# Kernel tuning notes

Measured on AMD Instinct MI355X. Metric: run time of the kernel, lower is better.

Reference implementation:

```python
import jax, jax.numpy as jnp
import numpy as np

NUM_STEPS = 32
BETA = 0.9
THRESHOLD = 1.0   # LIF firing threshold
LAT_THR = 0.01    # snntorch spikegen.latency default threshold
EPS = 1e-7        # snntorch epsilon
SLOPE = 25.0      # fast_sigmoid surrogate slope
ENC_THR = 0.75    # SpikeEncoder latency_threshold

B, S, F_IN = 512, 64, 128
HIDDEN = [256, 256, 128]


def spike_fn(u):
    # Heaviside forward; surrogate grad handled in fwdbwd module. Forward-only here.
    return (u > 0).astype(u.dtype)


def latency_encode(x, num_steps):
    """SpikeEncoder('latency') -> snntorch.spikegen.latency, normalize=True, linear=False."""
    # gate small values
    x = jnp.where(x < ENC_THR, jnp.zeros_like(x), x)
    # per-channel min-max normalization over the sequence dim (dim=1)
    x_min = jnp.min(x, axis=1, keepdims=True)
    x_max = jnp.max(x, axis=1, keepdims=True)
    xn = (x - x_min) / (x_max - x_min + 1e-8)
    # logarithmic latency code (tau=1, first_spike_time=0, normalize=True)
    d = jnp.clip(xn, LAT_THR + EPS, None)
    t = jnp.log(d / (d - LAT_THR))
    t_max = np.log((LAT_THR + EPS) / EPS)  # spike time of smallest intensity
    t = t * (num_steps - 1) / np.float32(t_max)
    t_idx = jnp.clip(jnp.round(t), 0, num_steps - 1).astype(jnp.int32)  # (B,S,F)
    # one-hot over time -> (T, B, S, F), matches spikegen scatter
    steps = jnp.arange(num_steps, dtype=jnp.int32).reshape(-1, 1, 1, 1)
    return (steps == t_idx[None]).astype(jnp.float32)


def snn_block(x, W, b, beta, thr):
    """Linear over all timesteps, then LIF (reset-by-subtraction) via scan.
    x: (T, B, in) -> spk: (T, B, hidden)"""
    cur = jnp.einsum('tbi,hi->tbh', x, W) + b

    def step(mem, c):
        # snntorch Leaky: reset computed from previous mem (detached)
        reset = jax.lax.stop_gradient((mem - thr > 0).astype(mem.dtype))
        mem = beta * mem + c - reset * thr
        spk = spike_fn(mem - thr)
        return mem, spk

    mem0 = jnp.zeros(cur.shape[1:], cur.dtype)
    _, spk = jax.lax.scan(step, cur[0] * 0 + mem0, cur)
    return spk


def setup_inputs() -> dict:
    key = jax.random.key(0)
    ks = jax.random.split(key, 7)
    x = jax.random.normal(ks[0], (B, S, F_IN), dtype=jnp.float32)
    sizes = [F_IN] + HIDDEN
    params = {}
    for i in range(3):
        fan_in = sizes[i]
        bound = 1.0 / np.sqrt(fan_in)
        params[f'W{i+1}'] = jax.random.uniform(ks[2 * i + 1], (sizes[i + 1], fan_in),
                                               minval=-bound, maxval=bound, dtype=jnp.float32)
        params[f'b{i+1}'] = jax.random.uniform(ks[2 * i + 2], (sizes[i + 1],),
                                               minval=-bound, maxval=bound, dtype=jnp.float32)
    return {'x': x, **params}


def reference(x, W1, b1, W2, b2, W3, b3):
    spikes = latency_encode(x, NUM_STEPS)        # (T, B, S, F)
    spikes = spikes.mean(axis=2)                 # (T, B, F)
    spikes = snn_block(spikes, W1, b1, BETA, THRESHOLD)
    spikes = snn_block(spikes, W2, b2, BETA, THRESHOLD)
    spikes = snn_block(spikes, W3, b3, BETA, THRESHOLD)
    return spikes                                # (T, B, hidden_sizes[-1])
```

## Files before the change

kernel.cpp:

```cpp
#include <hip/hip_runtime.h>
#include <cstddef>

#define T_STEPS 32
#define B_SZ    512
#define S_SZ    64
#define F_INPUT 128
#define H1      256
#define H2      256
#define H3      128

typedef _Float16 half_t;
typedef __attribute__((ext_vector_type(8))) _Float16 half8;
typedef __attribute__((ext_vector_type(4))) float   float4v;

__device__ inline void split_store_sw(float w, half_t* out, int n, int k, int kchunks) {
    half_t hi = (half_t)w;
    float hif = (float)hi;
    if (fabsf(hif) < 6.103515625e-05f) { hi = (half_t)0.0f; hif = 0.0f; }
    half_t lo = (half_t)((w - hif) * 4096.0f);
    int n_tile = n >> 4, lr = n & 15;
    int k_chunk = k >> 5, kin = k & 31, quad = kin >> 3, j = kin & 7;
    size_t base = (size_t)(n_tile * kchunks + k_chunk) * 1024;
    size_t off  = base + (size_t)((quad << 4) + lr) * 8 + j;
    out[off]       = hi;
    out[off + 512] = lo;
}

__global__ __launch_bounds__(256)
void prep_w_kernel(const float* __restrict__ W1, const float* __restrict__ W2,
                   const float* __restrict__ W3,
                   half_t* __restrict__ ws1, half_t* __restrict__ ws2,
                   half_t* __restrict__ ws3) {
    int e = blockIdx.x * blockDim.x + threadIdx.x;
    if (e < H1 * F_INPUT) {
        split_store_sw(W1[e], ws1, e / F_INPUT, e % F_INPUT, F_INPUT / 32);
    } else if (e < H1 * F_INPUT + H2 * H1) {
        int i = e - H1 * F_INPUT;
        split_store_sw(W2[i], ws2, i / H1, i % H1, H1 / 32);
    } else {
        int i = e - H1 * F_INPUT - H2 * H1;
        split_store_sw(W3[i], ws3, i / H2, i % H2, H2 / 32);
    }
}

#define CUR_STRIDE 260
#define AS_STRIDE  136
#define SPK_STRIDE 264
#define SMEM_CUR   0
#define SMEM_AS    33280
#define SMEM_SPK   33280
#define SMEM_TOTAL 50176

template<int KCHUNKS, int NT, int ASTRIDE>
__device__ __forceinline__ void gemm_phase(const half_t* __restrict__ Wsw,
                                           const float*  __restrict__ bias,
                                           const half_t* __restrict__ Als,
                                           float* __restrict__ curT,
                                           int wave, int lane) {
    const int quad = lane >> 4, lr = lane & 15;
    float4v acc_h[2][NT], acc_l[2][NT];
#pragma unroll
    for (int mt = 0; mt < 2; ++mt)
#pragma unroll
        for (int nt = 0; nt < NT; ++nt) {
            acc_h[mt][nt] = (float4v){0.0f, 0.0f, 0.0f, 0.0f};
            acc_l[mt][nt] = (float4v){0.0f, 0.0f, 0.0f, 0.0f};
        }

    half8 wh[NT], wl[NT];
#pragma unroll
    for (int nt = 0; nt < NT; ++nt) {
        const half_t* p = Wsw + ((size_t)(wave * NT + nt) * KCHUNKS) * 1024 + lane * 8;
        wh[nt] = *(const half8*)(p);
        wl[nt] = *(const half8*)(p + 512);
    }

#pragma unroll
    for (int c = 0; c < KCHUNKS; ++c) {
        half8 a0 = *(const half8*)(Als + lr * ASTRIDE        + c * 32 + quad * 8);
        half8 a1 = *(const half8*)(Als + (16 + lr) * ASTRIDE + c * 32 + quad * 8);
        half8 nwh[NT], nwl[NT];
        if (c + 1 < KCHUNKS) {
#pragma unroll
            for (int nt = 0; nt < NT; ++nt) {
                const half_t* p =
                    Wsw + ((size_t)(wave * NT + nt) * KCHUNKS + c + 1) * 1024 + lane * 8;
                nwh[nt] = *(const half8*)(p);
                nwl[nt] = *(const half8*)(p + 512);
            }
        }
#pragma unroll
        for (int nt = 0; nt < NT; ++nt) {
            acc_h[0][nt] = __builtin_amdgcn_mfma_f32_16x16x32_f16(a0, wh[nt], acc_h[0][nt], 0, 0, 0);
            acc_h[1][nt] = __builtin_amdgcn_mfma_f32_16x16x32_f16(a1, wh[nt], acc_h[1][nt], 0, 0, 0);
            acc_l[0][nt] = __builtin_amdgcn_mfma_f32_16x16x32_f16(a0, wl[nt], acc_l[0][nt], 0, 0, 0);
            acc_l[1][nt] = __builtin_amdgcn_mfma_f32_16x16x32_f16(a1, wl[nt], acc_l[1][nt], 0, 0, 0);
        }
#pragma unroll
        for (int nt = 0; nt < NT; ++nt) { wh[nt] = nwh[nt]; wl[nt] = nwl[nt]; }
    }

#pragma unroll
    for (int nt = 0; nt < NT; ++nt) {
        int col = wave * NT * 16 + nt * 16 + lr;
        float bj = bias[col];
#pragma unroll
        for (int mt = 0; mt < 2; ++mt) {
            int rbase = mt * 16 + quad * 4;
#pragma unroll
            for (int r = 0; r < 4; ++r) {
                float v = acc_h[mt][nt][r] + 2.44140625e-04f * acc_l[mt][nt][r];
                curT[(rbase + r) * CUR_STRIDE + col] = v + bj;
            }
        }
    }
}

__global__ __launch_bounds__(512, 4)
void snn_mega_kernel(const float* __restrict__ x,
                     const half_t* __restrict__ ws1, const float* __restrict__ b1,
                     const half_t* __restrict__ ws2, const float* __restrict__ b2,
                     const half_t* __restrict__ ws3, const float* __restrict__ b3,
                     float* __restrict__ out) {
    __shared__ __align__(16) char smem[SMEM_TOTAL];
    float*  curT = (float*) (smem + SMEM_CUR);
    half_t* As   = (half_t*)(smem + SMEM_AS);
    half_t* spk  = (half_t*)(smem + SMEM_SPK);

    const int tid  = threadIdx.x;
    const int b    = blockIdx.x;
    const int wave = tid >> 6;
    const int lane = tid & 63;

    const int f  = tid & 127;
    const int sh = (tid >> 7) & 1;
    const float* xp = x + (size_t)b * (S_SZ * F_INPUT) + (size_t)sh * 32 * F_INPUT + f;
    float* scratch = curT;

    float v[32];
    if (tid < 256) {
#pragma unroll
        for (int s = 0; s < 32; ++s) {
            float val = xp[(size_t)s * F_INPUT];
            v[s] = (val < 0.75f) ? 0.0f : val;
        }
        float mn = 1e30f, mx = -1e30f;
#pragma unroll
        for (int s = 0; s < 32; ++s) {
            mn = fminf(mn, v[s]);
            mx = fmaxf(mx, v[s]);
        }
        scratch[sh * 128 + f]       = mn;
        scratch[256 + sh * 128 + f] = mx;
    }
    __syncthreads();
    float fmn = fminf(scratch[f], scratch[128 + f]);
    float fmx = fmaxf(scratch[256 + f], scratch[384 + f]);
    __syncthreads();

    if (tid < 256) {
        float* hist = scratch;
#pragma unroll
        for (int t = 0; t < T_STEPS; ++t) hist[sh * 4096 + t * 128 + f] = 0.0f;
        const float denom = fmx - fmn + 1e-8f;
#pragma unroll
        for (int s = 0; s < 32; ++s) {
            float g = v[s];
            float xn = (g - fmn) / denom;
            float d  = fmaxf(xn, 0.0100001f);
            float tt = logf(d / (d - 0.01f));
            tt = tt * 31.0f;
            tt = tt / 11.512935464920229f;
            float tr = rintf(tt);
            tr = fminf(fmaxf(tr, 0.0f), 31.0f);
            hist[sh * 4096 + (int)tr * 128 + f] += 1.0f;
        }
    }
    __syncthreads();

#pragma unroll
    for (int i = 0; i < 8; ++i) {
        int idx = tid + i * 512;
        int t = idx >> 7, ff = idx & 127;
        float cnt = scratch[t * 128 + ff] + scratch[4096 + t * 128 + ff];
        As[t * AS_STRIDE + ff] = (half_t)(cnt * 0.015625f);
    }
    __syncthreads();

    gemm_phase<F_INPUT / 32, 2, AS_STRIDE>(ws1, b1, As, curT, wave, lane);
    __syncthreads();
    if (tid < 256) {
#pragma clang fp contract(off)
        const int h = tid;
        float mem = 0.0f;
#pragma unroll
        for (int t = 0; t < T_STEPS; ++t) {
            float c = curT[t * CUR_STRIDE + h];
            float reset = (mem - 1.0f > 0.0f) ? 1.0f : 0.0f;
            float p = 0.9f * mem;
            p = p + c;
            mem = p - reset;
            spk[t * SPK_STRIDE + h] = (half_t)((mem - 1.0f > 0.0f) ? 1.0f : 0.0f);
        }
    }
    __syncthreads();

    gemm_phase<H1 / 32, 2, SPK_STRIDE>(ws2, b2, spk, curT, wave, lane);
    __syncthreads();
    if (tid < 256) {
#pragma clang fp contract(off)
        const int h = tid;
        float mem = 0.0f;
#pragma unroll
        for (int t = 0; t < T_STEPS; ++t) {
            float c = curT[t * CUR_STRIDE + h];
            float reset = (mem - 1.0f > 0.0f) ? 1.0f : 0.0f;
            float p = 0.9f * mem;
            p = p + c;
            mem = p - reset;
            spk[t * SPK_STRIDE + h] = (half_t)((mem - 1.0f > 0.0f) ? 1.0f : 0.0f);
        }
    }
    __syncthreads();

    gemm_phase<H2 / 32, 1, SPK_STRIDE>(ws3, b3, spk, curT, wave, lane);
    __syncthreads();
    if (tid < H3) {
#pragma clang fp contract(off)
        const int h = tid;
        float mem = 0.0f;
#pragma unroll
        for (int t = 0; t < T_STEPS; ++t) {
            float c = curT[t * CUR_STRIDE + h];
            float reset = (mem - 1.0f > 0.0f) ? 1.0f : 0.0f;
            float p = 0.9f * mem;
            p = p + c;
            mem = p - reset;
            out[((size_t)t * B_SZ + b) * H3 + h] = (mem - 1.0f > 0.0f) ? 1.0f : 0.0f;
        }
    }
}

extern "C" void kernel_launch(void* const* d_in, const int* in_sizes, int n_in,
                              void* d_out, int out_size, void* d_ws, size_t ws_size,
                              hipStream_t stream) {
    const float* x  = (const float*)d_in[0];
    const float* W1 = (const float*)d_in[1];
    const float* b1 = (const float*)d_in[2];
    const float* W2 = (const float*)d_in[3];
    const float* b2 = (const float*)d_in[4];
    const float* W3 = (const float*)d_in[5];
    const float* b3 = (const float*)d_in[6];
    float* out = (float*)d_out;

    char* ws = (char*)d_ws;
    half_t* ws1 = (half_t*)ws;
    half_t* ws2 = (half_t*)(ws + 128 * 1024);
    half_t* ws3 = (half_t*)(ws + 384 * 1024);

    prep_w_kernel<<<(H1 * F_INPUT + H2 * H1 + H3 * H2) / 256, 256, 0, stream>>>(
        W1, W2, W3, ws1, ws2, ws3);

    snn_mega_kernel<<<B_SZ, 512, 0, stream>>>(x, ws1, b1, ws2, b2, ws3, b3, out);
}
```

Baseline: 96.83 us.

## Split fused mega-kernel into encode and per-layer GEMM+LIF kernels

Replaces the single per-batch mega-kernel with an encode kernel plus three GEMM+LIF kernels. Each GEMM kernel splits the hidden dimension across two blocks, so layers 1 and 2 launch twice as many blocks, and it uses smaller shared-memory tiles. The goal is more parallelism and occupancy and fewer idle threads in the LIF and encode phases. In exchange it adds kernel-launch overhead and global-memory round trips for the rates and spike tensors between layers.

After: 111.4 us. +15.0%, slower.

```diff
diff --git a/kernel.cpp b/kernel.cpp
--- a/kernel.cpp
+++ b/kernel.cpp
@@ -43,67 +43,141 @@
     }
 }
 
-#define CUR_STRIDE 260
-#define AS_STRIDE  136
-#define SPK_STRIDE 264
-#define SMEM_CUR   0
-#define SMEM_AS    33280
-#define SMEM_SPK   33280
-#define SMEM_TOTAL 50176
-
-template<int KCHUNKS, int NT, int ASTRIDE>
-__device__ __forceinline__ void gemm_phase(const half_t* __restrict__ Wsw,
-                                           const float*  __restrict__ bias,
-                                           const half_t* __restrict__ Als,
-                                           float* __restrict__ curT,
-                                           int wave, int lane) {
+__global__ __launch_bounds__(256)
+void encode_kernel(const float* __restrict__ x, half_t* __restrict__ rates) {
+    __shared__ float scratch[8192];
+    const int tid = threadIdx.x;
+    const int b   = blockIdx.x;
+    const int f   = tid & 127;
+    const int sh  = tid >> 7;
+    const float* xp = x + (size_t)b * (S_SZ * F_INPUT) + (size_t)sh * 32 * F_INPUT + f;
+
+    float v[32];
+#pragma unroll
+    for (int s = 0; s < 32; ++s) {
+        float val = xp[(size_t)s * F_INPUT];
+        v[s] = (val < 0.75f) ? 0.0f : val;
+    }
+    float mn = 1e30f, mx = -1e30f;
+#pragma unroll
+    for (int s = 0; s < 32; ++s) {
+        mn = fminf(mn, v[s]);
+        mx = fmaxf(mx, v[s]);
+    }
+    scratch[sh * 128 + f]       = mn;
+    scratch[256 + sh * 128 + f] = mx;
+    __syncthreads();
+    float fmn = fminf(scratch[f], scratch[128 + f]);
+    float fmx = fmaxf(scratch[256 + f], scratch[384 + f]);
+    __syncthreads();
+
+#pragma unroll
+    for (int t = 0; t < T_STEPS; ++t) scratch[sh * 4096 + t * 128 + f] = 0.0f;
+    const float denom = fmx - fmn + 1e-8f;
+#pragma unroll
+    for (int s = 0; s < 32; ++s) {
+        float g  = v[s];
+        float xn = (g - fmn) / denom;
+        float d  = fmaxf(xn, 0.0100001f);
+        float tt = logf(d / (d - 0.01f));
+        tt = tt * 31.0f;
+        tt = tt / 11.512935464920229f;
+        float tr = rintf(tt);
+        tr = fminf(fmaxf(tr, 0.0f), 31.0f);
+        scratch[sh * 4096 + (int)tr * 128 + f] += 1.0f;
+    }
+    __syncthreads();
+
+#pragma unroll
+    for (int i = 0; i < 16; ++i) {
+        int idx = tid + i * 256;
+        int t = idx >> 7, ff = idx & 127;
+        float cnt = scratch[t * 128 + ff] + scratch[4096 + t * 128 + ff];
+        rates[((size_t)b * T_STEPS + t) * F_INPUT + ff] = (half_t)(cnt * 0.015625f);
+    }
+}
+
+#define CUR_STRIDE 132
+#define SMEM_AS_MAX 16896
+#define SMEM_GEMM  (SMEM_AS_MAX + 32 * CUR_STRIDE * 4)
+
+template<int KCH, int FINAL>
+__global__ __launch_bounds__(256)
+void gemm_lif(const half_t* __restrict__ A,
+              const half_t* __restrict__ Wsw,
+              const float*  __restrict__ bias,
+              half_t* __restrict__ spk_next,
+              float*  __restrict__ out_final,
+              int Nfull) {
+    constexpr int K = KCH * 32;
+    constexpr int ASTRIDE = K + 8;
+    __shared__ __align__(16) char smem[SMEM_GEMM];
+    half_t* As   = (half_t*)smem;
+    float*  curT = (float*)(smem + SMEM_AS_MAX);
+
+    const int tid  = threadIdx.x;
+    const int b    = blockIdx.x;
+    const int n0   = blockIdx.y * 128;
+    const int wave = tid >> 6;
+    const int lane = tid & 63;
     const int quad = lane >> 4, lr = lane & 15;
-    float4v acc_h[2][NT], acc_l[2][NT];
+
+#pragma unroll
+    for (int i = 0; i < KCH / 2; ++i) {
+        int idx  = i * 256 + tid;
+        int row  = idx / (KCH * 4);
+        int colh = (idx % (KCH * 4)) * 8;
+        *(uint4*)(&As[row * ASTRIDE + colh]) =
+            *(const uint4*)(A + ((size_t)b * 32 + row) * K + colh);
+    }
+    __syncthreads();
+
+    float4v acc_h[2][2], acc_l[2][2];
 #pragma unroll
     for (int mt = 0; mt < 2; ++mt)
 #pragma unroll
-        for (int nt = 0; nt < NT; ++nt) {
+        for (int nt = 0; nt < 2; ++nt) {
             acc_h[mt][nt] = (float4v){0.0f, 0.0f, 0.0f, 0.0f};
             acc_l[mt][nt] = (float4v){0.0f, 0.0f, 0.0f, 0.0f};
         }
-
-    half8 wh[NT], wl[NT];
-#pragma unroll
-    for (int nt = 0; nt < NT; ++nt) {
-        const half_t* p = Wsw + ((size_t)(wave * NT + nt) * KCHUNKS) * 1024 + lane * 8;
+    const int ntile0 = (n0 >> 4) + wave * 2;
+
+    half8 wh[2], wl[2];
+#pragma unroll
+    for (int nt = 0; nt < 2; ++nt) {
+        const half_t* p = Wsw + ((size_t)(ntile0 + nt) * KCH) * 1024 + lane * 8;
         wh[nt] = *(const half8*)(p);
         wl[nt] = *(const half8*)(p + 512);
     }
-
-#pragma unroll
-    for (int c = 0; c < KCHUNKS; ++c) {
-        half8 a0 = *(const half8*)(Als + lr * ASTRIDE        + c * 32 + quad * 8);
-        half8 a1 = *(const half8*)(Als + (16 + lr) * ASTRIDE + c * 32 + quad * 8);
-        half8 nwh[NT], nwl[NT];
-        if (c + 1 < KCHUNKS) {
-#pragma unroll
-            for (int nt = 0; nt < NT; ++nt) {
+#pragma unroll
+    for (int c = 0; c < KCH; ++c) {
+        half8 a0 = *(const half8*)(&As[lr * ASTRIDE        + c * 32 + quad * 8]);
+        half8 a1 = *(const half8*)(&As[(16 + lr) * ASTRIDE + c * 32 + quad * 8]);
+        half8 nwh[2], nwl[2];
+        if (c + 1 < KCH) {
+#pragma unroll
+            for (int nt = 0; nt < 2; ++nt) {
                 const half_t* p =
-                    Wsw + ((size_t)(wave * NT + nt) * KCHUNKS + c + 1) * 1024 + lane * 8;
+                    Wsw + ((size_t)(ntile0 + nt) * KCH + c + 1) * 1024 + lane * 8;
                 nwh[nt] = *(const half8*)(p);
                 nwl[nt] = *(const half8*)(p + 512);
             }
         }
 #pragma unroll
-        for (int nt = 0; nt < NT; ++nt) {
+        for (int nt = 0; nt < 2; ++nt) {
             acc_h[0][nt] = __builtin_amdgcn_mfma_f32_16x16x32_f16(a0, wh[nt], acc_h[0][nt], 0, 0, 0);
             acc_h[1][nt] = __builtin_amdgcn_mfma_f32_16x16x32_f16(a1, wh[nt], acc_h[1][nt], 0, 0, 0);
             acc_l[0][nt] = __builtin_amdgcn_mfma_f32_16x16x32_f16(a0, wl[nt], acc_l[0][nt], 0, 0, 0);
             acc_l[1][nt] = __builtin_amdgcn_mfma_f32_16x16x32_f16(a1, wl[nt], acc_l[1][nt], 0, 0, 0);
         }
 #pragma unroll
-        for (int nt = 0; nt < NT; ++nt) { wh[nt] = nwh[nt]; wl[nt] = nwl[nt]; }
-    }
-
-#pragma unroll
-    for (int nt = 0; nt < NT; ++nt) {
-        int col = wave * NT * 16 + nt * 16 + lr;
-        float bj = bias[col];
+        for (int nt = 0; nt < 2; ++nt) { wh[nt] = nwh[nt]; wl[nt] = nwl[nt]; }
+    }
+
+#pragma unroll
+    for (int nt = 0; nt < 2; ++nt) {
+        int col = (wave * 2 + nt) * 16 + lr;
+        float bj = bias[n0 + col];
 #pragma unroll
         for (int mt = 0; mt < 2; ++mt) {
             int rbase = mt * 16 + quad * 4;
@@ -114,82 +188,9 @@
             }
         }
     }
-}
-
-__global__ __launch_bounds__(512, 4)
-void snn_mega_kernel(const float* __restrict__ x,
-                     const half_t* __restrict__ ws1, const float* __restrict__ b1,
-                     const half_t* __restrict__ ws2, const float* __restrict__ b2,
-                     const half_t* __restrict__ ws3, const float* __restrict__ b3,
-                     float* __restrict__ out) {
-    __shared__ __align__(16) char smem[SMEM_TOTAL];
-    float*  curT = (float*) (smem + SMEM_CUR);
-    half_t* As   = (half_t*)(smem + SMEM_AS);
-    half_t* spk  = (half_t*)(smem + SMEM_SPK);
-
-    const int tid  = threadIdx.x;
-    const int b    = blockIdx.x;
-    const int wave = tid >> 6;
-    const int lane = tid & 63;
-
-    const int f  = tid & 127;
-    const int sh = (tid >> 7) & 1;
-    const float* xp = x + (size_t)b * (S_SZ * F_INPUT) + (size_t)sh * 32 * F_INPUT + f;
-    float* scratch = curT;
-
-    float v[32];
-    if (tid < 256) {
-#pragma unroll
-        for (int s = 0; s < 32; ++s) {
-            float val = xp[(size_t)s * F_INPUT];
-            v[s] = (val < 0.75f) ? 0.0f : val;
-        }
-        float mn = 1e30f, mx = -1e30f;
-#pragma unroll
-        for (int s = 0; s < 32; ++s) {
-            mn = fminf(mn, v[s]);
-            mx = fmaxf(mx, v[s]);
-        }
-        scratch[sh * 128 + f]       = mn;
-        scratch[256 + sh * 128 + f] = mx;
-    }
-    __syncthreads();
-    float fmn = fminf(scratch[f], scratch[128 + f]);
-    float fmx = fmaxf(scratch[256 + f], scratch[384 + f]);
-    __syncthreads();
-
-    if (tid < 256) {
-        float* hist = scratch;
-#pragma unroll
-        for (int t = 0; t < T_STEPS; ++t) hist[sh * 4096 + t * 128 + f] = 0.0f;
-        const float denom = fmx - fmn + 1e-8f;
-#pragma unroll
-        for (int s = 0; s < 32; ++s) {
-            float g = v[s];
-            float xn = (g - fmn) / denom;
-            float d  = fmaxf(xn, 0.0100001f);
-            float tt = logf(d / (d - 0.01f));
-            tt = tt * 31.0f;
-            tt = tt / 11.512935464920229f;
-            float tr = rintf(tt);
-            tr = fminf(fmaxf(tr, 0.0f), 31.0f);
-            hist[sh * 4096 + (int)tr * 128 + f] += 1.0f;
-        }
-    }
-    __syncthreads();
-
-#pragma unroll
-    for (int i = 0; i < 8; ++i) {
-        int idx = tid + i * 512;
-        int t = idx >> 7, ff = idx & 127;
-        float cnt = scratch[t * 128 + ff] + scratch[4096 + t * 128 + ff];
-        As[t * AS_STRIDE + ff] = (half_t)(cnt * 0.015625f);
-    }
-    __syncthreads();
-
-    gemm_phase<F_INPUT / 32, 2, AS_STRIDE>(ws1, b1, As, curT, wave, lane);
-    __syncthreads();
-    if (tid < 256) {
+    __syncthreads();
+
+    if (tid < 128) {
 #pragma clang fp contract(off)
         const int h = tid;
         float mem = 0.0f;
@@ -200,43 +201,12 @@
             float p = 0.9f * mem;
             p = p + c;
             mem = p - reset;
-            spk[t * SPK_STRIDE + h] = (half_t)((mem - 1.0f > 0.0f) ? 1.0f : 0.0f);
-        }
-    }
-    __syncthreads();
-
-    gemm_phase<H1 / 32, 2, SPK_STRIDE>(ws2, b2, spk, curT, wave, lane);
-    __syncthreads();
-    if (tid < 256) {
-#pragma clang fp contract(off)
-        const int h = tid;
-        float mem = 0.0f;
-#pragma unroll
-        for (int t = 0; t < T_STEPS; ++t) {
-            float c = curT[t * CUR_STRIDE + h];
-            float reset = (mem - 1.0f > 0.0f) ? 1.0f : 0.0f;
-            float p = 0.9f * mem;
-            p = p + c;
-            mem = p - reset;
-            spk[t * SPK_STRIDE + h] = (half_t)((mem - 1.0f > 0.0f) ? 1.0f : 0.0f);
-        }
-    }
-    __syncthreads();
-
-    gemm_phase<H2 / 32, 1, SPK_STRIDE>(ws3, b3, spk, curT, wave, lane);
-    __syncthreads();
-    if (tid < H3) {
-#pragma clang fp contract(off)
-        const int h = tid;
-        float mem = 0.0f;
-#pragma unroll
-        for (int t = 0; t < T_STEPS; ++t) {
-            float c = curT[t * CUR_STRIDE + h];
-            float reset = (mem - 1.0f > 0.0f) ? 1.0f : 0.0f;
-            float p = 0.9f * mem;
-            p = p + c;
-            mem = p - reset;
-            out[((size_t)t * B_SZ + b) * H3 + h] = (mem - 1.0f > 0.0f) ? 1.0f : 0.0f;
+            float s = (mem - 1.0f > 0.0f) ? 1.0f : 0.0f;
+            if (FINAL) {
+                out_final[((size_t)t * B_SZ + b) * H3 + h] = s;
+            } else {
+                spk_next[((size_t)b * T_STEPS + t) * Nfull + n0 + h] = (half_t)s;
+            }
         }
     }
 }
@@ -254,12 +224,24 @@
     float* out = (float*)d_out;
 
     char* ws = (char*)d_ws;
-    half_t* ws1 = (half_t*)ws;
-    half_t* ws2 = (half_t*)(ws + 128 * 1024);
-    half_t* ws3 = (half_t*)(ws + 384 * 1024);
+    half_t* ws1   = (half_t*)ws;
+    half_t* ws2   = (half_t*)(ws + 128 * 1024);
+    half_t* ws3   = (half_t*)(ws + 384 * 1024);
+    half_t* rates = (half_t*)(ws + (size_t) 1 * 1024 * 1024);
+    half_t* spk1  = (half_t*)(ws + (size_t) 5 * 1024 * 1024);
+    half_t* spk2  = (half_t*)(ws + (size_t)13 * 1024 * 1024);
 
     prep_w_kernel<<<(H1 * F_INPUT + H2 * H1 + H3 * H2) / 256, 256, 0, stream>>>(
         W1, W2, W3, ws1, ws2, ws3);
 
-    snn_mega_kernel<<<B_SZ, 512, 0, stream>>>(x, ws1, b1, ws2, b2, ws3, b3, out);
-}
+    encode_kernel<<<B_SZ, 256, 0, stream>>>(x, rates);
+
+    gemm_lif<4, 0><<<dim3(B_SZ, 2), 256, 0, stream>>>(
+        rates, ws1, b1, spk1, nullptr, H1);
+
+    gemm_lif<8, 0><<<dim3(B_SZ, 2), 256, 0, stream>>>(
+        spk1, ws2, b2, spk2, nullptr, H2);
+
+    gemm_lif<8, 1><<<dim3(B_SZ, 1), 256, 0, stream>>>(
+        spk2, ws3, b3, nullptr, out, H3);
+}
```

## Fuse LIF scan into each wave's GEMM epilogue and drop barriers

Applied to the files above, without the earlier changes.

Each wave now runs the LIF recurrence over the columns it just wrote, so the block-wide barrier between each GEMM and its scan goes away. Separate ping-pong spike buffers (spkA/spkB) replace the single shared spike buffer, and shared memory grows from about 49KB to about 74KB. With larger LDS use, fewer blocks may fit per CU. Only 32 or 16 lanes per wave do the serial scan, so lane utilization during the scan is low.

Measured after the change: 97.08 us. About the same (+0.3%).

```diff
diff --git a/kernel.cpp b/kernel.cpp
--- a/kernel.cpp
+++ b/kernel.cpp
@@ -43,20 +43,23 @@
     }
 }
 
-#define CUR_STRIDE 260
 #define AS_STRIDE  136
 #define SPK_STRIDE 264
-#define SMEM_CUR   0
-#define SMEM_AS    33280
-#define SMEM_SPK   33280
-#define SMEM_TOTAL 50176
-
-template<int KCHUNKS, int NT, int ASTRIDE>
-__device__ __forceinline__ void gemm_phase(const half_t* __restrict__ Wsw,
-                                           const float*  __restrict__ bias,
-                                           const half_t* __restrict__ Als,
-                                           float* __restrict__ curT,
-                                           int wave, int lane) {
+#define CUR_STRIDE 260
+#define SMEM_AS    0
+#define SMEM_CUR   8704
+#define SMEM_SPKA  41984
+#define SMEM_SPKB  58880
+#define SMEM_TOTAL 75776
+
+template<int KCHUNKS, int NT, int ASTRIDE, int FINAL>
+__device__ __forceinline__ void gemm_lif_wave(const half_t* __restrict__ Wsw,
+                                              const float*  __restrict__ bias,
+                                              const half_t* __restrict__ Als,
+                                              float*  __restrict__ curT,
+                                              half_t* __restrict__ spk_out,
+                                              float*  __restrict__ out_final,
+                                              int b, int wave, int lane) {
     const int quad = lane >> 4, lr = lane & 15;
     float4v acc_h[2][NT], acc_l[2][NT];
 #pragma unroll
@@ -74,11 +77,12 @@
         wh[nt] = *(const half8*)(p);
         wl[nt] = *(const half8*)(p + 512);
     }
-
 #pragma unroll
     for (int c = 0; c < KCHUNKS; ++c) {
-        half8 a0 = *(const half8*)(Als + lr * ASTRIDE        + c * 32 + quad * 8);
-        half8 a1 = *(const half8*)(Als + (16 + lr) * ASTRIDE + c * 32 + quad * 8);
+        half8 a[2];
+#pragma unroll
+        for (int mt = 0; mt < 2; ++mt)
+            a[mt] = *(const half8*)(Als + (mt * 16 + lr) * ASTRIDE + c * 32 + quad * 8);
         half8 nwh[NT], nwl[NT];
         if (c + 1 < KCHUNKS) {
 #pragma unroll
@@ -90,19 +94,19 @@
             }
         }
 #pragma unroll
-        for (int nt = 0; nt < NT; ++nt) {
-            acc_h[0][nt] = __builtin_amdgcn_mfma_f32_16x16x32_f16(a0, wh[nt], acc_h[0][nt], 0, 0, 0);
-            acc_h[1][nt] = __builtin_amdgcn_mfma_f32_16x16x32_f16(a1, wh[nt], acc_h[1][nt], 0, 0, 0);
-            acc_l[0][nt] = __builtin_amdgcn_mfma_f32_16x16x32_f16(a0, wl[nt], acc_l[0][nt], 0, 0, 0);
-            acc_l[1][nt] = __builtin_amdgcn_mfma_f32_16x16x32_f16(a1, wl[nt], acc_l[1][nt], 0, 0, 0);
-        }
+        for (int nt = 0; nt < NT; ++nt)
+#pragma unroll
+            for (int mt = 0; mt < 2; ++mt) {
+                acc_h[mt][nt] = __builtin_amdgcn_mfma_f32_16x16x32_f16(a[mt], wh[nt], acc_h[mt][nt], 0, 0, 0);
+                acc_l[mt][nt] = __builtin_amdgcn_mfma_f32_16x16x32_f16(a[mt], wl[nt], acc_l[mt][nt], 0, 0, 0);
+            }
 #pragma unroll
         for (int nt = 0; nt < NT; ++nt) { wh[nt] = nwh[nt]; wl[nt] = nwl[nt]; }
     }
 
 #pragma unroll
     for (int nt = 0; nt < NT; ++nt) {
-        int col = wave * NT * 16 + nt * 16 + lr;
+        int col = (wave * NT + nt) * 16 + lr;
         float bj = bias[col];
 #pragma unroll
         for (int mt = 0; mt < 2; ++mt) {
@@ -111,6 +115,26 @@
             for (int r = 0; r < 4; ++r) {
                 float v = acc_h[mt][nt][r] + 2.44140625e-04f * acc_l[mt][nt][r];
                 curT[(rbase + r) * CUR_STRIDE + col] = v + bj;
+            }
+        }
+    }
+
+    if (lane < NT * 16) {
+#pragma clang fp contract(off)
+        const int col = wave * NT * 16 + lane;
+        float mem = 0.0f;
+#pragma unroll
+        for (int t = 0; t < T_STEPS; ++t) {
+            float c = curT[t * CUR_STRIDE + col];
+            float reset = (mem - 1.0f > 0.0f) ? 1.0f : 0.0f;
+            float p = 0.9f * mem;
+            p = p + c;
+            mem = p - reset;
+            float s = (mem - 1.0f > 0.0f) ? 1.0f : 0.0f;
+            if (FINAL) {
+                out_final[((size_t)t * B_SZ + b) * H3 + col] = s;
+            } else {
+                spk_out[t * SPK_STRIDE + col] = (half_t)s;
             }
         }
     }
@@ -123,9 +147,11 @@
                      const half_t* __restrict__ ws3, const float* __restrict__ b3,
                      float* __restrict__ out) {
     __shared__ __align__(16) char smem[SMEM_TOTAL];
+    half_t* As   = (half_t*)(smem + SMEM_AS);
     float*  curT = (float*) (smem + SMEM_CUR);
-    half_t* As   = (half_t*)(smem + SMEM_AS);
-    half_t* spk  = (half_t*)(smem + SMEM_SPK);
+    half_t* spkA = (half_t*)(smem + SMEM_SPKA);
+    half_t* spkB = (half_t*)(smem + SMEM_SPKB);
+    float*  scratch = (float*)(smem + SMEM_CUR);
 
     const int tid  = threadIdx.x;
     const int b    = blockIdx.x;
@@ -135,9 +161,9 @@
     const int f  = tid & 127;
     const int sh = (tid >> 7) & 1;
     const float* xp = x + (size_t)b * (S_SZ * F_INPUT) + (size_t)sh * 32 * F_INPUT + f;
-    float* scratch = curT;
 
     float v[32];
+    float fmn = 0.0f, fmx = 0.0f;
     if (tid < 256) {
 #pragma unroll
         for (int s = 0; s < 32; ++s) {
@@ -154,8 +180,10 @@
         scratch[256 + sh * 128 + f] = mx;
     }
     __syncthreads();
-    float fmn = fminf(scratch[f], scratch[128 + f]);
-    float fmx = fmaxf(scratch[256 + f], scratch[384 + f]);
+    if (tid < 256) {
+        fmn = fminf(scratch[f], scratch[128 + f]);
+        fmx = fmaxf(scratch[256 + f], scratch[384 + f]);
+    }
     __syncthreads();
 
     if (tid < 256) {
@@ -165,7 +193,7 @@
         const float denom = fmx - fmn + 1e-8f;
 #pragma unroll
         for (int s = 0; s < 32; ++s) {
-            float g = v[s];
+            float g  = v[s];
             float xn = (g - fmn) / denom;
             float d  = fmaxf(xn, 0.0100001f);
             float tt = logf(d / (d - 0.01f));
@@ -178,67 +206,27 @@
     }
     __syncthreads();
 
-#pragma unroll
-    for (int i = 0; i < 8; ++i) {
-        int idx = tid + i * 512;
-        int t = idx >> 7, ff = idx & 127;
-        float cnt = scratch[t * 128 + ff] + scratch[4096 + t * 128 + ff];
-        As[t * AS_STRIDE + ff] = (half_t)(cnt * 0.015625f);
-    }
-    __syncthreads();
-
-    gemm_phase<F_INPUT / 32, 2, AS_STRIDE>(ws1, b1, As, curT, wave, lane);
-    __syncthreads();
-    if (tid < 256) {
-#pragma clang fp contract(off)
-        const int h = tid;
-        float mem = 0.0f;
-#pragma unroll
-        for (int t = 0; t < T_STEPS; ++t) {
-            float c = curT[t * CUR_STRIDE + h];
-            float reset = (mem - 1.0f > 0.0f) ? 1.0f : 0.0f;
-            float p = 0.9f * mem;
-            p = p + c;
-            mem = p - reset;
-            spk[t * SPK_STRIDE + h] = (half_t)((mem - 1.0f > 0.0f) ? 1.0f : 0.0f);
-        }
-    }
-    __syncthreads();
-
-    gemm_phase<H1 / 32, 2, SPK_STRIDE>(ws2, b2, spk, curT, wave, lane);
-    __syncthreads();
-    if (tid < 256) {
-#pragma clang fp contract(off)
-        const int h = tid;
-        float mem = 0.0f;
-#pragma unroll
-        for (int t = 0; t < T_STEPS; ++t) {
-            float c = curT[t * CUR_STRIDE + h];
-            float reset = (mem - 1.0f > 0.0f) ? 1.0f : 0.0f;
-            float p = 0.9f * mem;
-            p = p + c;
-            mem = p - reset;
-            spk[t * SPK_STRIDE + h] = (half_t)((mem - 1.0f > 0.0f) ? 1.0f : 0.0f);
-        }
-    }
-    __syncthreads();
-
-    gemm_phase<H2 / 32, 1, SPK_STRIDE>(ws3, b3, spk, curT, wave, lane);
-    __syncthreads();
-    if (tid < H3) {
-#pragma clang fp contract(off)
-        const int h = tid;
-        float mem = 0.0f;
-#pragma unroll
-        for (int t = 0; t < T_STEPS; ++t) {
-            float c = curT[t * CUR_STRIDE + h];
-            float reset = (mem - 1.0f > 0.0f) ? 1.0f : 0.0f;
-            float p = 0.9f * mem;
-            p = p + c;
-            mem = p - reset;
-            out[((size_t)t * B_SZ + b) * H3 + h] = (mem - 1.0f > 0.0f) ? 1.0f : 0.0f;
-        }
-    }
+    if (tid < 256) {
+#pragma unroll
+        for (int i = 0; i < 16; ++i) {
+            int idx = tid + i * 256;
+            int t = idx >> 7, ff = idx & 127;
+            float cnt = scratch[t * 128 + ff] + scratch[4096 + t * 128 + ff];
+            As[t * AS_STRIDE + ff] = (half_t)(cnt * 0.015625f);
+        }
+    }
+    __syncthreads();
+
+    gemm_lif_wave<F_INPUT / 32, 2, AS_STRIDE, 0>(ws1, b1, As, curT, spkA, nullptr,
+                                                 b, wave, lane);
+    __syncthreads();
+
+    gemm_lif_wave<H1 / 32, 2, SPK_STRIDE, 0>(ws2, b2, spkA, curT, spkB, nullptr,
+                                             b, wave, lane);
+    __syncthreads();
+
+    gemm_lif_wave<H2 / 32, 1, SPK_STRIDE, 1>(ws3, b3, spkB, curT, nullptr, out,
+                                             b, wave, lane);
 }
 
 extern "C" void kernel_launch(void* const* d_in, const int* in_sizes, int n_in,
```
